# Kernel optimization log

Measured on AMD Instinct MI355X. Metric: run time of the kernel, lower is better.

## Reference

```python
import math
import jax, jax.numpy as jnp
import numpy as np

NUM_SUPERPIXELS = 256
COMPACTNESS = 10.0
NUM_ITERATIONS = 5


def _cdist(a, b):
    # Euclidean pairwise distance: a [B,N,C], b [B,K,C] -> [B,N,K]
    a2 = jnp.sum(a * a, axis=-1)[:, :, None]
    b2 = jnp.sum(b * b, axis=-1)[:, None, :]
    ab = jnp.einsum('bnc,bkc->bnk', a, b)
    return jnp.sqrt(jnp.maximum(a2 + b2 - 2.0 * ab, 1e-12))


def setup_inputs() -> dict:
    key = jax.random.key(0)
    x = jax.random.normal(key, (4, 200, 128, 128), dtype=jnp.float32)
    return {"x": x}


def reference(x):
    B, C, H, W = x.shape
    N = H * W

    # --- initialize_centers (grid of seed pixels, taken from x[0]) ---
    grid_h = int(math.sqrt(NUM_SUPERPIXELS * H / W))
    grid_w = NUM_SUPERPIXELS // grid_h
    K = grid_h * grid_w
    h_step, w_step = H // grid_h, W // grid_w
    h_idx = jnp.arange(h_step // 2, H, h_step)[:grid_h]
    w_idx = jnp.arange(w_step // 2, W, w_step)[:grid_w]
    gy, gx = jnp.meshgrid(h_idx, w_idx, indexing='ij')
    init_spatial = jnp.stack([gy.flatten(), gx.flatten()], axis=1).astype(jnp.float32)  # [K,2]
    flat_idx = gy.flatten() * W + gx.flatten()  # [K]

    # --- pixel coordinates ---
    yg, xg = jnp.meshgrid(jnp.arange(H), jnp.arange(W), indexing='ij')
    pix = jnp.stack([yg.flatten(), xg.flatten()], axis=1).astype(jnp.float32)  # [N,2]
    pix_b = jnp.broadcast_to(pix[None], (B, N, 2))

    x_flat = jnp.transpose(x, (0, 2, 3, 1)).reshape(B, N, C)  # [B,N,C]
    centers_spectral = jnp.broadcast_to(x_flat[0][flat_idx][None], (B, K, C))
    centers_spatial = jnp.broadcast_to(init_spatial[None], (B, K, 2))

    S = math.sqrt(H * W / NUM_SUPERPIXELS)
    Q = None
    for _ in range(NUM_ITERATIONS):
        D = _cdist(x_flat, centers_spectral) + (COMPACTNESS / S) * _cdist(pix_b, centers_spatial)
        Q = jax.nn.softmax(-D, axis=-1)  # [B,N,K]
        mass = jnp.sum(Q, axis=1)[:, :, None] + 1e-06  # [B,K,1]
        centers_spectral = jnp.einsum('bnk,bnc->bkc', Q, x_flat) / mass
        centers_spatial = jnp.einsum('bnk,bnc->bkc', Q, pix_b) / mass
    return Q, centers_spectral
```

## Files before the change

kernel.cpp:

```cpp
#include <hip/hip_runtime.h>
#include <math.h>

#define B 4
#define C 200
#define H 128
#define W 128
#define N 16384
#define K 256
#define ITERS 5
#define FACT 1.25f
#define NT 32
#define NTM 128
#define CPAD 208
#define CP2  224

typedef __attribute__((ext_vector_type(8))) __bf16 bf16x8;
typedef __attribute__((ext_vector_type(4))) float f32x4;

#define OFF_A2    0
#define OFF_CS    (OFF_A2 + B*N)
#define OFF_CSPAT (OFF_CS + B*K*C)
#define OFF_B2    (OFF_CSPAT + B*K*2)
#define OFF_SACC  (OFF_B2 + B*K)
#define OFF_MACC  (OFF_SACC + B*K*C)
#define OFF_SPACC (OFF_MACC + B*K)
#define OFF_CST   (OFF_SPACC + B*K*2)
#define CST_SZ    (B*C*K)
#define OFF_PART  (OFF_CST + CST_SZ)
#define PART_SZ   (B*NT*CPAD*K)
#define OFF_MPART (OFF_PART + PART_SZ)
#define MPART_SZ  (B*NTM*3*K)
#define WS_NEED   ((size_t)(OFF_MPART + MPART_SZ) * 4)
#define OFF_XBF   (OFF_MPART + MPART_SZ)
#define XBF_SZF   (B*N*CP2/2)
#define OFF_CSBF  (OFF_XBF + XBF_SZF)
#define CSBF_SZF  (B*K*CP2/2)
#define WS_NEED2  ((size_t)(OFF_CSBF + CSBF_SZF) * 4)

__global__ void k_init(const float* __restrict__ x, float* __restrict__ cs,
                       __bf16* __restrict__ csbf, float* __restrict__ cspat,
                       int fast) {
  int k = blockIdx.x, c = threadIdx.x;
  int i = k >> 4, j = k & 15;
  int sn = (4 + 8*i)*W + (4 + 8*j);
  if (c < C) {
    float v = x[(size_t)c*N + sn];
    for (int b = 0; b < B; ++b) {
      cs[((size_t)(b*K + k))*C + c] = v;
      if (fast) csbf[((size_t)(b*K + k))*CP2 + c] = (__bf16)v;
    }
  } else if (fast && c < CP2) {
    for (int b = 0; b < B; ++b)
      csbf[((size_t)(b*K + k))*CP2 + c] = (__bf16)0.f;
  }
  if (c == 0) {
    for (int b = 0; b < B; ++b) {
      cspat[(b*K + k)*2 + 0] = (float)(4 + 8*i);
      cspat[(b*K + k)*2 + 1] = (float)(4 + 8*j);
    }
  }
}

__global__ __launch_bounds__(256) void k_prep(const float* __restrict__ x,
                                              __bf16* __restrict__ xbf) {
  __shared__ float xt[32*64];
  int bid = blockIdx.x;
  int b  = bid >> 8;
  int n0 = (bid & 255) << 6;
  int tid = threadIdx.x;
  const float* xb = x + (size_t)b*C*N;
  __bf16* xo = xbf + ((size_t)b*N + n0)*CP2;
  for (int t = 0; t < 7; ++t) {
    int cc0 = t*32;
    __syncthreads();
    #pragma unroll
    for (int pass = 0; pass < 2; ++pass) {
      int f = pass*256 + tid;
      int ci = f >> 4, nq = f & 15;
      float4 v = make_float4(0.f, 0.f, 0.f, 0.f);
      if (cc0 + ci < C) v = *(const float4*)&xb[(size_t)(cc0 + ci)*N + n0 + nq*4];
      *(float4*)&xt[ci*64 + nq*4] = v;
    }
    __syncthreads();
    {
      int n = tid & 63, cg8 = (tid >> 6) * 8;
      bf16x8 pk;
      #pragma unroll
      for (int i = 0; i < 8; ++i) pk[i] = (__bf16)xt[(cg8 + i)*64 + n];
      *(bf16x8*)&xo[(size_t)n*CP2 + cc0 + cg8] = pk;
    }
  }
}

__global__ void k_a2(const float* __restrict__ x, float* __restrict__ a2) {
  int b = blockIdx.x >> 6;
  int n = ((blockIdx.x & 63) << 8) + threadIdx.x;
  const float* xp = x + (size_t)b*C*N + n;
  float s = 0.f;
  #pragma unroll 8
  for (int c = 0; c < C; ++c) { float v = xp[(size_t)c*N]; s += v*v; }
  a2[b*N + n] = s;
}

__global__ void k_b2(const float* __restrict__ cs, float* __restrict__ b2) {
  int bk = blockIdx.x;
  const float* p = cs + (size_t)bk*C;
  float s = 0.f;
  for (int c = threadIdx.x; c < C; c += 64) { float v = p[c]; s += v*v; }
  for (int off = 32; off > 0; off >>= 1) s += __shfl_down(s, off);
  if (threadIdx.x == 0) b2[bk] = s;
}

__global__ __launch_bounds__(512, 2) void k_assign2(
    const __bf16* __restrict__ xbf, const __bf16* __restrict__ csbf,
    const float* __restrict__ cspat, const float* __restrict__ b2,
    const float* __restrict__ a2, float* __restrict__ Q) {
  __shared__ float b2s[K], cys[K], cxs[K];
  __shared__ float a2s[128];
  __shared__ float redw[8*128];
  __shared__ float redf[128];

  int b   = blockIdx.x >> 7;
  int n0  = (blockIdx.x & 127) << 7;
  int tid = threadIdx.x;
  int lane = tid & 63;
  int lr = lane & 15;
  int lg = lane >> 4;
  int w  = tid >> 6;

  if (tid < K) {
    b2s[tid] = b2[b*K + tid];
    cys[tid] = cspat[(b*K + tid)*2 + 0];
    cxs[tid] = cspat[(b*K + tid)*2 + 1];
  }
  if (tid < 128) a2s[tid] = a2[b*N + n0 + tid];
  __syncthreads();

  f32x4 acc[16];
  #pragma unroll
  for (int i = 0; i < 16; ++i) acc[i] = (f32x4){0.f, 0.f, 0.f, 0.f};

  const __bf16* cb = csbf + ((size_t)b*K + (size_t)(w*32 + lr))*CP2;
  const __bf16* xb = xbf + ((size_t)(b*N + n0 + lr))*CP2;

  for (int t = 0; t < 7; ++t) {
    int cc = t*32 + lg*8;
    bf16x8 b0 = *(const bf16x8*)&cb[cc];
    bf16x8 b1 = *(const bf16x8*)&cb[(size_t)16*CP2 + cc];
    #pragma unroll
    for (int nt = 0; nt < 8; ++nt) {
      bf16x8 av = *(const bf16x8*)&xb[(size_t)(nt*16)*CP2 + cc];
      acc[nt*2+0] = __builtin_amdgcn_mfma_f32_16x16x32_bf16(av, b0, acc[nt*2+0], 0, 0, 0);
      acc[nt*2+1] = __builtin_amdgcn_mfma_f32_16x16x32_bf16(av, b1, acc[nt*2+1], 0, 0, 0);
    }
  }

  float py = (float)(n0 >> 7);
  int k0 = w*32 + lr, k1 = k0 + 16;
  float b2v0 = b2s[k0], b2v1 = b2s[k1];
  float cx0 = cxs[k0], cx1 = cxs[k1];
  float dy0 = py - cys[k0], dy1 = py - cys[k1];
  float dyy0 = dy0*dy0, dyy1 = dy1*dy1;

  float mArr[32];
  #pragma unroll
  for (int nt = 0; nt < 8; ++nt) {
    #pragma unroll
    for (int r = 0; r < 4; ++r) {
      int pix = nt*16 + lg*4 + r;
      float a2v = a2s[pix];
      float pxv = (float)pix;
      float dx0 = pxv - cx0, dx1 = pxv - cx1;
      float d0 = sqrtf(fmaxf(a2v + b2v0 - 2.f*acc[nt*2+0][r], 1e-12f))
               + FACT*sqrtf(fmaxf(dyy0 + dx0*dx0, 1e-12f));
      float d1 = sqrtf(fmaxf(a2v + b2v1 - 2.f*acc[nt*2+1][r], 1e-12f))
               + FACT*sqrtf(fmaxf(dyy1 + dx1*dx1, 1e-12f));
      float e0 = __expf(-d0);
      float e1 = __expf(-d1);
      acc[nt*2+0][r] = e0;
      acc[nt*2+1][r] = e1;
      float s = e0 + e1;
      s += __shfl_xor(s, 1);
      s += __shfl_xor(s, 2);
      s += __shfl_xor(s, 4);
      s += __shfl_xor(s, 8);
      mArr[nt*4+r] = s;
    }
  }
  if (lr == 0) {
    #pragma unroll
    for (int nt = 0; nt < 8; ++nt)
      #pragma unroll
      for (int r = 0; r < 4; ++r)
        redw[w*128 + nt*16 + lg*4 + r] = mArr[nt*4+r];
  }
  __syncthreads();
  if (tid < 128) {
    float s = redw[tid];
    #pragma unroll
    for (int g = 1; g < 8; ++g) s += redw[g*128 + tid];
    redf[tid] = 1.f / s;
  }
  __syncthreads();
  float* Qb = Q + ((size_t)(b*N + n0))*K;
  #pragma unroll
  for (int nt = 0; nt < 8; ++nt) {
    #pragma unroll
    for (int r = 0; r < 4; ++r) {
      int pix = nt*16 + lg*4 + r;
      float inv = redf[pix];
      Qb[(size_t)pix*K + k0] = acc[nt*2+0][r] * inv;
      Qb[(size_t)pix*K + k1] = acc[nt*2+1][r] * inv;
    }
  }
}

__global__ __launch_bounds__(512, 2) void k_assign(
    const float* __restrict__ x, const float* __restrict__ cs,
    const float* __restrict__ cspat, const float* __restrict__ b2,
    const float* __restrict__ a2, float* __restrict__ Q) {
  __shared__ __bf16 cs_lds[K*40];
  __shared__ __bf16 x_lds[128*40];
  __shared__ float b2s[K], cys[K], cxs[K];
  __shared__ float a2s[128];
  __shared__ float redw[8*128];
  __shared__ float redf[128];

  int b   = blockIdx.x >> 7;
  int n0  = (blockIdx.x & 127) << 7;
  int tid = threadIdx.x;
  int lane = tid & 63;
  int lr = lane & 15;
  int lg = lane >> 4;
  int w  = tid >> 6;

  if (tid < K) {
    b2s[tid] = b2[b*K + tid];
    cys[tid] = cspat[(b*K + tid)*2 + 0];
    cxs[tid] = cspat[(b*K + tid)*2 + 1];
  }
  if (tid < 128) a2s[tid] = a2[b*N + n0 + tid];

  f32x4 acc[16];
  #pragma unroll
  for (int i = 0; i < 16; ++i) acc[i] = (f32x4){0.f, 0.f, 0.f, 0.f};

  const float* xb = x + (size_t)b*C*N;
  const float* cb = cs + (size_t)b*K*C;

  for (int t = 0; t < 7; ++t) {
    int cc0 = t * 32;
    __syncthreads();
    #pragma unroll
    for (int pass = 0; pass < 4; ++pass) {
      int f = pass*512 + tid;
      int k = f >> 3, c4 = (f & 7) * 4;
      float4 v = make_float4(0.f, 0.f, 0.f, 0.f);
      if (cc0 + c4 < 200) v = *(const float4*)&cb[(size_t)k*C + cc0 + c4];
      __bf16* d = &cs_lds[k*40 + c4];
      d[0] = (__bf16)v.x; d[1] = (__bf16)v.y;
      d[2] = (__bf16)v.z; d[3] = (__bf16)v.w;
    }
    #pragma unroll
    for (int pass = 0; pass < 8; ++pass) {
      int idx = pass*512 + tid;
      int ci = idx >> 7, p = idx & 127;
      float xv = (cc0 + ci < 200) ? xb[(size_t)(cc0 + ci)*N + n0 + p] : 0.f;
      x_lds[p*40 + ci] = (__bf16)xv;
    }
    __syncthreads();
    const __bf16* bbase = &cs_lds[(w*32 + lr)*40 + lg*8];
    bf16x8 b0 = *(const bf16x8*)bbase;
    bf16x8 b1 = *(const bf16x8*)(bbase + 16*40);
    const __bf16* abase = &x_lds[lr*40 + lg*8];
    #pragma unroll
    for (int nt = 0; nt < 8; ++nt) {
      bf16x8 av = *(const bf16x8*)(abase + nt*16*40);
      acc[nt*2+0] = __builtin_amdgcn_mfma_f32_16x16x32_bf16(av, b0, acc[nt*2+0], 0, 0, 0);
      acc[nt*2+1] = __builtin_amdgcn_mfma_f32_16x16x32_bf16(av, b1, acc[nt*2+1], 0, 0, 0);
    }
  }

  float py = (float)(n0 >> 7);
  float mArr[32];
  #pragma unroll
  for (int nt = 0; nt < 8; ++nt) {
    #pragma unroll
    for (int r = 0; r < 4; ++r) {
      int pix = nt*16 + lg*4 + r;
      float a2v = a2s[pix];
      float pxv = (float)pix;
      float dmin = 1e30f;
      #pragma unroll
      for (int j = 0; j < 2; ++j) {
        int k = w*32 + j*16 + lr;
        float ab = acc[nt*2+j][r];
        float dy = py - cys[k];
        float dx = pxv - cxs[k];
        float d = sqrtf(fmaxf(a2v + b2s[k] - 2.f*ab, 1e-12f))
                + FACT*sqrtf(fmaxf(dy*dy + dx*dx, 1e-12f));
        acc[nt*2+j][r] = d;
        dmin = fminf(dmin, d);
      }
      mArr[nt*4+r] = dmin;
    }
  }
  #pragma unroll
  for (int i = 0; i < 32; ++i) {
    float m = mArr[i];
    m = fminf(m, __shfl_xor(m, 1));
    m = fminf(m, __shfl_xor(m, 2));
    m = fminf(m, __shfl_xor(m, 4));
    m = fminf(m, __shfl_xor(m, 8));
    mArr[i] = m;
  }
  if (lr == 0) {
    #pragma unroll
    for (int nt = 0; nt < 8; ++nt)
      #pragma unroll
      for (int r = 0; r < 4; ++r)
        redw[w*128 + nt*16 + lg*4 + r] = mArr[nt*4+r];
  }
  __syncthreads();
  if (tid < 128) {
    float m = redw[tid];
    #pragma unroll
    for (int g = 1; g < 8; ++g) m = fminf(m, redw[g*128 + tid]);
    redf[tid] = m;
  }
  __syncthreads();
  #pragma unroll
  for (int nt = 0; nt < 8; ++nt) {
    #pragma unroll
    for (int r = 0; r < 4; ++r) {
      int pix = nt*16 + lg*4 + r;
      float mnv = redf[pix];
      float s = 0.f;
      #pragma unroll
      for (int j = 0; j < 2; ++j) {
        float e = __expf(mnv - acc[nt*2+j][r]);
        acc[nt*2+j][r] = e;
        s += e;
      }
      s += __shfl_xor(s, 1);
      s += __shfl_xor(s, 2);
      s += __shfl_xor(s, 4);
      s += __shfl_xor(s, 8);
      mArr[nt*4+r] = s;
    }
  }
  if (lr == 0) {
    #pragma unroll
    for (int nt = 0; nt < 8; ++nt)
      #pragma unroll
      for (int r = 0; r < 4; ++r)
        redw[w*128 + nt*16 + lg*4 + r] = mArr[nt*4+r];
  }
  __syncthreads();
  if (tid < 128) {
    float s = redw[tid];
    #pragma unroll
    for (int g = 1; g < 8; ++g) s += redw[g*128 + tid];
    redf[tid] = 1.f / s;
  }
  __syncthreads();
  float* Qb = Q + ((size_t)(b*N + n0))*K;
  #pragma unroll
  for (int nt = 0; nt < 8; ++nt) {
    #pragma unroll
    for (int r = 0; r < 4; ++r) {
      int pix = nt*16 + lg*4 + r;
      float inv = redf[pix];
      #pragma unroll
      for (int j = 0; j < 2; ++j) {
        int k = w*32 + j*16 + lr;
        Qb[(size_t)pix*K + k] = acc[nt*2+j][r] * inv;
      }
    }
  }
}

__global__ __launch_bounds__(256) void k_update4(
    const float* __restrict__ x, const float* __restrict__ Q,
    float* __restrict__ part) {
  __shared__ float  q32[32*256];
  __shared__ __bf16 qbf[256*40];
  __shared__ __bf16 xbf[64*40];
  int bid = blockIdx.x;
  int b   = bid >> 7;
  int rem = bid & 127;
  int cg  = rem >> 5;
  int nt  = rem & 31;
  int tid = threadIdx.x;
  int lane = tid & 63, lr = lane & 15, lg = lane >> 4;
  int w   = tid >> 6;
  int c0  = cg * 64;

  f32x4 acc[16];
  #pragma unroll
  for (int i = 0; i < 16; ++i) acc[i] = (f32x4){0.f, 0.f, 0.f, 0.f};

  const float* Qb = Q + (size_t)b*N*K;
  const float* xb = x + (size_t)b*C*N;

  for (int ch = 0; ch < 16; ++ch) {
    int nb = nt*512 + ch*32;
    __syncthreads();
    #pragma unroll
    for (int pass = 0; pass < 8; ++pass) {
      int f = pass*256 + tid;
      int n = f >> 6, k4 = f & 63;
      *(float4*)&q32[n*256 + k4*4] =
          *(const float4*)&Qb[(size_t)(nb + n)*K + k4*4];
    }
    #pragma unroll
    for (int pass = 0; pass < 2; ++pass) {
      int f = pass*256 + tid;
      int c = f >> 3, n4 = f & 7;
      int cc = c0 + c;
      float4 v = make_float4(0.f, 0.f, 0.f, 0.f);
      if (cc < 200) v = *(const float4*)&xb[(size_t)cc*N + nb + n4*4];
      __bf16* d = &xbf[c*40 + n4*4];
      d[0] = (__bf16)v.x; d[1] = (__bf16)v.y;
      d[2] = (__bf16)v.z; d[3] = (__bf16)v.w;
    }
    __syncthreads();
    {
      #pragma unroll
      for (int g = 0; g < 4; ++g) {
        bf16x8 pk;
        #pragma unroll
        for (int i = 0; i < 8; ++i)
          pk[i] = (__bf16)q32[(g*8 + i)*256 + tid];
        *(bf16x8*)&qbf[tid*40 + g*8] = pk;
      }
    }
    __syncthreads();
    const __bf16* abase = &qbf[(w*64 + lr)*40 + lg*8];
    const __bf16* bbase = &xbf[lr*40 + lg*8];
    bf16x8 A0 = *(const bf16x8*)(abase);
    bf16x8 A1 = *(const bf16x8*)(abase + 16*40);
    bf16x8 A2 = *(const bf16x8*)(abase + 32*40);
    bf16x8 A3 = *(const bf16x8*)(abase + 48*40);
    bf16x8 B0 = *(const bf16x8*)(bbase);
    bf16x8 B1 = *(const bf16x8*)(bbase + 16*40);
    bf16x8 B2 = *(const bf16x8*)(bbase + 32*40);
    bf16x8 B3 = *(const bf16x8*)(bbase + 48*40);
    acc[0]  = __builtin_amdgcn_mfma_f32_16x16x32_bf16(A0, B0, acc[0], 0, 0, 0);
    acc[1]  = __builtin_amdgcn_mfma_f32_16x16x32_bf16(A0, B1, acc[1], 0, 0, 0);
    acc[2]  = __builtin_amdgcn_mfma_f32_16x16x32_bf16(A0, B2, acc[2], 0, 0, 0);
    acc[3]  = __builtin_amdgcn_mfma_f32_16x16x32_bf16(A0, B3, acc[3], 0, 0, 0);
    acc[4]  = __builtin_amdgcn_mfma_f32_16x16x32_bf16(A1, B0, acc[4], 0, 0, 0);
    acc[5]  = __builtin_amdgcn_mfma_f32_16x16x32_bf16(A1, B1, acc[5], 0, 0, 0);
    acc[6]  = __builtin_amdgcn_mfma_f32_16x16x32_bf16(A1, B2, acc[6], 0, 0, 0);
    acc[7]  = __builtin_amdgcn_mfma_f32_16x16x32_bf16(A1, B3, acc[7], 0, 0, 0);
    acc[8]  = __builtin_amdgcn_mfma_f32_16x16x32_bf16(A2, B0, acc[8], 0, 0, 0);
    acc[9]  = __builtin_amdgcn_mfma_f32_16x16x32_bf16(A2, B1, acc[9], 0, 0, 0);
    acc[10] = __builtin_amdgcn_mfma_f32_16x16x32_bf16(A2, B2, acc[10], 0, 0, 0);
    acc[11] = __builtin_amdgcn_mfma_f32_16x16x32_bf16(A2, B3, acc[11], 0, 0, 0);
    acc[12] = __builtin_amdgcn_mfma_f32_16x16x32_bf16(A3, B0, acc[12], 0, 0, 0);
    acc[13] = __builtin_amdgcn_mfma_f32_16x16x32_bf16(A3, B1, acc[13], 0, 0, 0);
    acc[14] = __builtin_amdgcn_mfma_f32_16x16x32_bf16(A3, B2, acc[14], 0, 0, 0);
    acc[15] = __builtin_amdgcn_mfma_f32_16x16x32_bf16(A3, B3, acc[15], 0, 0, 0);
  }

  float* pp = part + (size_t)(b*NT + nt) * CPAD * K;
  #pragma unroll
  for (int t = 0; t < 4; ++t) {
    #pragma unroll
    for (int u = 0; u < 4; ++u) {
      int c = c0 + u*16 + lr;
      if (c < CPAD) {
        int k = w*64 + t*16 + lg*4;
        *(f32x4*)&pp[(size_t)c*K + k] = acc[t*4+u];
      }
    }
  }
}

__global__ __launch_bounds__(256) void k_mass(
    const float* __restrict__ Q, float* __restrict__ mpart) {
  int bid = blockIdx.x;
  int b = bid >> 7, nt = bid & 127;
  int tid = threadIdx.x;
  const float* Qb = Q + (size_t)b*N*K;
  int nbase = nt * 128;
  float mass = 0.f, sy = 0.f, sx = 0.f;
  for (int nn = 0; nn < 128; nn += 8) {
    float qv[8];
    #pragma unroll
    for (int j = 0; j < 8; ++j)
      qv[j] = Qb[(size_t)(nbase + nn + j)*K + tid];
    #pragma unroll
    for (int j = 0; j < 8; ++j) {
      int n = nbase + nn + j;
      mass += qv[j];
      sy += qv[j] * (float)(n >> 7);
      sx += qv[j] * (float)(n & 127);
    }
  }
  float* mp = mpart + (size_t)(b*NTM + nt) * 3 * K;
  mp[tid]       = mass;
  mp[K + tid]   = sy;
  mp[2*K + tid] = sx;
}

__global__ __launch_bounds__(256) void k_reduce(
    const float* __restrict__ part, const float* __restrict__ mpart,
    float* __restrict__ sacc, float* __restrict__ macc,
    float* __restrict__ spacc) {
  int bid = blockIdx.x;
  int b = bid / 200;
  int c = bid % 200;
  int tid = threadIdx.x;
  float s = 0.f;
  for (int nt = 0; nt < NT; ++nt)
    s += part[((size_t)(b*NT + nt)*CPAD + c)*K + tid];
  sacc[(size_t)(b*K + tid)*C + c] = s;
  if (c == 0) {
    float m = 0.f, yy = 0.f, xx = 0.f;
    for (int nt = 0; nt < NTM; ++nt) {
      const float* mp = mpart + (size_t)(b*NTM + nt) * 3 * K;
      m  += mp[tid];
      yy += mp[K + tid];
      xx += mp[2*K + tid];
    }
    macc[b*K + tid] = m;
    spacc[(b*K + tid)*2 + 0] = yy;
    spacc[(b*K + tid)*2 + 1] = xx;
  }
}

__global__ __launch_bounds__(256, 2) void k_update(
    const float* __restrict__ x, const float* __restrict__ Q,
    float* __restrict__ sacc, float* __restrict__ macc,
    float* __restrict__ spacc) {
  __shared__ float x_lds[32*28];
  int bid = blockIdx.x;
  int b = bid >> 9;
  int rest = bid & 511;
  int ct = rest >> 6;
  int nt = rest & 63;
  int tid = threadIdx.x;
  int c0 = ct * 25;

  float acc[25];
  #pragma unroll
  for (int c = 0; c < 25; ++c) acc[c] = 0.f;
  float mass = 0.f, sy = 0.f, sx = 0.f;

  const float* xb = x + (size_t)b*C*N + (size_t)c0*N;
  const float* Qb = Q + (size_t)b*N*K;

  for (int ch = 0; ch < 8; ++ch) {
    int nb = nt*256 + ch*32;
    __syncthreads();
    #pragma unroll
    for (int pass = 0; pass < 4; ++pass) {
      int idx = pass*256 + tid;
      if (idx < 800) {
        int ci = idx >> 5, nn = idx & 31;
        x_lds[nn*28 + ci] = xb[(size_t)ci*N + nb + nn];
      }
    }
    __syncthreads();
    float py  = (float)(nb >> 7);
    float pxb = (float)(nb & 127);
    #pragma unroll
    for (int n4 = 0; n4 < 8; ++n4) {
      float qv[4];
      #pragma unroll
      for (int j = 0; j < 4; ++j)
        qv[j] = Qb[(size_t)(nb + n4*4 + j)*K + tid];
      #pragma unroll
      for (int j = 0; j < 4; ++j) {
        int nn = n4*4 + j;
        float q = qv[j];
        if (ct == 0) {
          mass += q;
          sy += q * py;
          sx += q * (pxb + (float)nn);
        }
        const float* xr = &x_lds[nn*28];
        #pragma unroll
        for (int c4 = 0; c4 < 6; ++c4) {
          float4 xv = *(const float4*)&xr[c4*4];
          acc[c4*4+0] = fmaf(q, xv.x, acc[c4*4+0]);
          acc[c4*4+1] = fmaf(q, xv.y, acc[c4*4+1]);
          acc[c4*4+2] = fmaf(q, xv.z, acc[c4*4+2]);
          acc[c4*4+3] = fmaf(q, xv.w, acc[c4*4+3]);
        }
        acc[24] = fmaf(q, xr[24], acc[24]);
      }
    }
  }
  float* sp = sacc + ((size_t)(b*K + tid))*C + c0;
  #pragma unroll
  for (int c = 0; c < 25; ++c) atomicAdd(&sp[c], acc[c]);
  if (ct == 0) {
    atomicAdd(&macc[b*K + tid], mass);
    atomicAdd(&spacc[(b*K + tid)*2 + 0], sy);
    atomicAdd(&spacc[(b*K + tid)*2 + 1], sx);
  }
}

__global__ void k_final(const float* __restrict__ sacc, const float* __restrict__ macc,
                        const float* __restrict__ spacc, float* __restrict__ cs,
                        __bf16* __restrict__ csbf, float* __restrict__ cspat,
                        float* __restrict__ b2, float* __restrict__ outc,
                        int last, int fast) {
  __shared__ float red[256];
  int bk = blockIdx.x;
  int c = threadIdx.x;
  float inv = 1.f / (macc[bk] + 1e-6f);
  float v = 0.f;
  if (c < C) {
    v = sacc[(size_t)bk*C + c] * inv;
    cs[(size_t)bk*C + c] = v;
    if (fast) csbf[(size_t)bk*CP2 + c] = (__bf16)v;
    if (last) outc[(size_t)bk*C + c] = v;
  } else if (c == C) {
    cspat[bk*2 + 0] = spacc[bk*2 + 0] * inv;
  } else if (c == C + 1) {
    cspat[bk*2 + 1] = spacc[bk*2 + 1] * inv;
  }
  red[c] = v * v;
  __syncthreads();
  for (int off = 128; off > 0; off >>= 1) {
    if (c < off) red[c] += red[c + off];
    __syncthreads();
  }
  if (c == 0) b2[bk] = red[0];
}

extern "C" void kernel_launch(void* const* d_in, const int* in_sizes, int n_in,
                              void* d_out, int out_size, void* d_ws, size_t ws_size,
                              hipStream_t stream) {
  const float* x = (const float*)d_in[0];
  float* out = (float*)d_out;
  float* ws  = (float*)d_ws;
  float* a2    = ws + OFF_A2;
  float* cs    = ws + OFF_CS;
  float* cspat = ws + OFF_CSPAT;
  float* b2    = ws + OFF_B2;
  float* sacc  = ws + OFF_SACC;
  float* macc  = ws + OFF_MACC;
  float* spacc = ws + OFF_SPACC;
  float* part  = ws + OFF_PART;
  float* mpart = ws + OFF_MPART;
  __bf16* xbf  = (__bf16*)(ws + OFF_XBF);
  __bf16* csbf = (__bf16*)(ws + OFF_CSBF);
  float* outc  = out + (size_t)B*N*K;
  int split = (ws_size >= WS_NEED) ? 1 : 0;
  int fast  = (ws_size >= WS_NEED2) ? 1 : 0;

  hipLaunchKernelGGL(k_init, dim3(K), dim3(256), 0, stream, x, cs, csbf, cspat, fast);
  hipLaunchKernelGGL(k_a2, dim3(B*64), dim3(256), 0, stream, x, a2);
  hipLaunchKernelGGL(k_b2, dim3(B*K), dim3(64), 0, stream, cs, b2);
  if (fast)
    hipLaunchKernelGGL(k_prep, dim3(B*256), dim3(256), 0, stream, x, xbf);
  for (int it = 0; it < ITERS; ++it) {
    if (fast)
      hipLaunchKernelGGL(k_assign2, dim3(B*128), dim3(512), 0, stream,
                         xbf, csbf, cspat, b2, a2, out);
    else
      hipLaunchKernelGGL(k_assign, dim3(B*128), dim3(512), 0, stream,
                         x, cs, cspat, b2, a2, out);
    if (split) {
      hipLaunchKernelGGL(k_update4, dim3(B*4*NT), dim3(256), 0, stream,
                         x, out, part);
      hipLaunchKernelGGL(k_mass, dim3(B*NTM), dim3(256), 0, stream,
                         out, mpart);
      hipLaunchKernelGGL(k_reduce, dim3(B*200), dim3(256), 0, stream,
                         part, mpart, sacc, macc, spacc);
    } else {
      hipMemsetAsync(sacc, 0, (size_t)(B*K*C + B*K + B*K*2)*sizeof(float), stream);
      hipLaunchKernelGGL(k_update, dim3(B*512), dim3(256), 0, stream,
                         x, out, sacc, macc, spacc);
    }
    hipLaunchKernelGGL(k_final, dim3(B*K), dim3(256), 0, stream,
                       sacc, macc, spacc, cs, csbf, cspat, b2, outc,
                       (it == ITERS-1) ? 1 : 0, fast);
  }
}
```

Before: 624.4 us.

## Emit transposed bf16 Q from assign and feed a direct-load MFMA update kernel

The assign kernel now also writes a K-major bf16 copy of Q, and a new prep kernel converts x once into a channel-major bf16 buffer padded to CPAD. A new update kernel then runs the Q^T·x reduction with MFMA, loading operands straight from these pre-laid-out global buffers with no LDS staging or on-the-fly conversion. This is meant to cut the fp32 read and convert cost of the update step. In exchange it adds extra workspace and extra bf16 stores in assign, and the new path only runs if the workspace is large enough.

```diff
diff --git a/kernel.cpp b/kernel.cpp
--- a/kernel.cpp
+++ b/kernel.cpp
@@ -15,6 +15,7 @@
 #define CP2  224
 
 typedef __attribute__((ext_vector_type(8))) __bf16 bf16x8;
+typedef __attribute__((ext_vector_type(4))) __bf16 bf16x4;
 typedef __attribute__((ext_vector_type(4))) float f32x4;
 
 #define OFF_A2    0
@@ -36,6 +37,11 @@
 #define OFF_CSBF  (OFF_XBF + XBF_SZF)
 #define CSBF_SZF  (B*K*CP2/2)
 #define WS_NEED2  ((size_t)(OFF_CSBF + CSBF_SZF) * 4)
+#define OFF_QTB   (OFF_CSBF + CSBF_SZF)
+#define QTB_SZF   (B*K*N/2)
+#define OFF_XB2   (OFF_QTB + QTB_SZF)
+#define XB2_SZF   (B*CPAD*N/2)
+#define WS_NEED3  ((size_t)(OFF_XB2 + XB2_SZF) * 4)
 
 __global__ void k_init(const float* __restrict__ x, float* __restrict__ cs,
                        __bf16* __restrict__ csbf, float* __restrict__ cspat,
@@ -92,6 +98,28 @@
   }
 }
 
+__global__ __launch_bounds__(256) void k_prep2(const float* __restrict__ x,
+                                               __bf16* __restrict__ xbf2) {
+  int g = blockIdx.x * 256 + threadIdx.x;
+  int per_b = CPAD * (N/8);
+  int b = g / per_b;
+  int rem = g - b*per_b;
+  int c = rem / (N/8);
+  int n = (rem - c*(N/8)) * 8;
+  bf16x8 pk;
+  if (c < C) {
+    const float* src = &x[((size_t)b*C + c)*N + n];
+    float4 v0 = *(const float4*)&src[0];
+    float4 v1 = *(const float4*)&src[4];
+    pk[0]=(__bf16)v0.x; pk[1]=(__bf16)v0.y; pk[2]=(__bf16)v0.z; pk[3]=(__bf16)v0.w;
+    pk[4]=(__bf16)v1.x; pk[5]=(__bf16)v1.y; pk[6]=(__bf16)v1.z; pk[7]=(__bf16)v1.w;
+  } else {
+    #pragma unroll
+    for (int i = 0; i < 8; ++i) pk[i] = (__bf16)0.f;
+  }
+  *(bf16x8*)&xbf2[((size_t)b*CPAD + c)*N + n] = pk;
+}
+
 __global__ void k_a2(const float* __restrict__ x, float* __restrict__ a2) {
   int b = blockIdx.x >> 6;
   int n = ((blockIdx.x & 63) << 8) + threadIdx.x;
@@ -114,7 +142,8 @@
 __global__ __launch_bounds__(512, 2) void k_assign2(
     const __bf16* __restrict__ xbf, const __bf16* __restrict__ csbf,
     const float* __restrict__ cspat, const float* __restrict__ b2,
-    const float* __restrict__ a2, float* __restrict__ Q) {
+    const float* __restrict__ a2, float* __restrict__ Q,
+    __bf16* __restrict__ qtb, int wq) {
   __shared__ float b2s[K], cys[K], cxs[K];
   __shared__ float a2s[128];
   __shared__ float redw[8*128];
@@ -203,14 +232,25 @@
   }
   __syncthreads();
   float* Qb = Q + ((size_t)(b*N + n0))*K;
+  __bf16* qt0 = qtb + ((size_t)b*K + k0)*N + n0;
+  __bf16* qt1 = qtb + ((size_t)b*K + k1)*N + n0;
   #pragma unroll
   for (int nt = 0; nt < 8; ++nt) {
+    bf16x4 p0, p1;
     #pragma unroll
     for (int r = 0; r < 4; ++r) {
       int pix = nt*16 + lg*4 + r;
       float inv = redf[pix];
-      Qb[(size_t)pix*K + k0] = acc[nt*2+0][r] * inv;
-      Qb[(size_t)pix*K + k1] = acc[nt*2+1][r] * inv;
+      float f0 = acc[nt*2+0][r] * inv;
+      float f1 = acc[nt*2+1][r] * inv;
+      Qb[(size_t)pix*K + k0] = f0;
+      Qb[(size_t)pix*K + k1] = f1;
+      p0[r] = (__bf16)f0;
+      p1[r] = (__bf16)f1;
+    }
+    if (wq) {
+      *(bf16x4*)&qt0[nt*16 + lg*4] = p0;
+      *(bf16x4*)&qt1[nt*16 + lg*4] = p1;
     }
   }
 }
@@ -375,6 +415,75 @@
       for (int j = 0; j < 2; ++j) {
         int k = w*32 + j*16 + lr;
         Qb[(size_t)pix*K + k] = acc[nt*2+j][r] * inv;
+      }
+    }
+  }
+}
+
+__global__ __launch_bounds__(256) void k_update5(
+    const __bf16* __restrict__ qtb, const __bf16* __restrict__ xbf2,
+    float* __restrict__ part) {
+  int bid = blockIdx.x;
+  int b   = bid >> 7;
+  int rem = bid & 127;
+  int cg  = rem >> 5;
+  int nt  = rem & 31;
+  int tid = threadIdx.x;
+  int lane = tid & 63, lr = lane & 15, lg = lane >> 4;
+  int w   = tid >> 6;
+  int c0  = cg * 64;
+
+  f32x4 acc[16];
+  #pragma unroll
+  for (int i = 0; i < 16; ++i) acc[i] = (f32x4){0.f, 0.f, 0.f, 0.f};
+
+  const __bf16* qb = qtb + ((size_t)b*K + (size_t)(w*64 + lr))*N;
+  int cr0 = c0 + lr;
+  int cr1 = min(c0 + 16 + lr, CPAD - 1);
+  int cr2 = min(c0 + 32 + lr, CPAD - 1);
+  int cr3 = min(c0 + 48 + lr, CPAD - 1);
+  const __bf16* xb0 = xbf2 + ((size_t)b*CPAD + cr0)*N;
+  const __bf16* xb1 = xbf2 + ((size_t)b*CPAD + cr1)*N;
+  const __bf16* xb2 = xbf2 + ((size_t)b*CPAD + cr2)*N;
+  const __bf16* xb3 = xbf2 + ((size_t)b*CPAD + cr3)*N;
+
+  for (int ch = 0; ch < 16; ++ch) {
+    int nb = nt*512 + ch*32 + lg*8;
+    bf16x8 A0 = *(const bf16x8*)&qb[nb];
+    bf16x8 A1 = *(const bf16x8*)&qb[(size_t)16*N + nb];
+    bf16x8 A2 = *(const bf16x8*)&qb[(size_t)32*N + nb];
+    bf16x8 A3 = *(const bf16x8*)&qb[(size_t)48*N + nb];
+    bf16x8 B0 = *(const bf16x8*)&xb0[nb];
+    bf16x8 B1 = *(const bf16x8*)&xb1[nb];
+    bf16x8 B2 = *(const bf16x8*)&xb2[nb];
+    bf16x8 B3 = *(const bf16x8*)&xb3[nb];
+    acc[0]  = __builtin_amdgcn_mfma_f32_16x16x32_bf16(A0, B0, acc[0], 0, 0, 0);
+    acc[1]  = __builtin_amdgcn_mfma_f32_16x16x32_bf16(A0, B1, acc[1], 0, 0, 0);
+    acc[2]  = __builtin_amdgcn_mfma_f32_16x16x32_bf16(A0, B2, acc[2], 0, 0, 0);
+    acc[3]  = __builtin_amdgcn_mfma_f32_16x16x32_bf16(A0, B3, acc[3], 0, 0, 0);
+    acc[4]  = __builtin_amdgcn_mfma_f32_16x16x32_bf16(A1, B0, acc[4], 0, 0, 0);
+    acc[5]  = __builtin_amdgcn_mfma_f32_16x16x32_bf16(A1, B1, acc[5], 0, 0, 0);
+    acc[6]  = __builtin_amdgcn_mfma_f32_16x16x32_bf16(A1, B2, acc[6], 0, 0, 0);
+    acc[7]  = __builtin_amdgcn_mfma_f32_16x16x32_bf16(A1, B3, acc[7], 0, 0, 0);
+    acc[8]  = __builtin_amdgcn_mfma_f32_16x16x32_bf16(A2, B0, acc[8], 0, 0, 0);
+    acc[9]  = __builtin_amdgcn_mfma_f32_16x16x32_bf16(A2, B1, acc[9], 0, 0, 0);
+    acc[10] = __builtin_amdgcn_mfma_f32_16x16x32_bf16(A2, B2, acc[10], 0, 0, 0);
+    acc[11] = __builtin_amdgcn_mfma_f32_16x16x32_bf16(A2, B3, acc[11], 0, 0, 0);
+    acc[12] = __builtin_amdgcn_mfma_f32_16x16x32_bf16(A3, B0, acc[12], 0, 0, 0);
+    acc[13] = __builtin_amdgcn_mfma_f32_16x16x32_bf16(A3, B1, acc[13], 0, 0, 0);
+    acc[14] = __builtin_amdgcn_mfma_f32_16x16x32_bf16(A3, B2, acc[14], 0, 0, 0);
+    acc[15] = __builtin_amdgcn_mfma_f32_16x16x32_bf16(A3, B3, acc[15], 0, 0, 0);
+  }
+
+  float* pp = part + (size_t)(b*NT + nt) * CPAD * K;
+  #pragma unroll
+  for (int t = 0; t < 4; ++t) {
+    #pragma unroll
+    for (int u = 0; u < 4; ++u) {
+      int c = c0 + u*16 + lr;
+      if (c < CPAD) {
+        int k = w*64 + t*16 + lg*4;
+        *(f32x4*)&pp[(size_t)c*K + k] = acc[t*4+u];
       }
     }
   }
@@ -650,25 +759,34 @@
   float* mpart = ws + OFF_MPART;
   __bf16* xbf  = (__bf16*)(ws + OFF_XBF);
   __bf16* csbf = (__bf16*)(ws + OFF_CSBF);
+  __bf16* qtb  = (__bf16*)(ws + OFF_QTB);
+  __bf16* xbf2 = (__bf16*)(ws + OFF_XB2);
   float* outc  = out + (size_t)B*N*K;
   int split = (ws_size >= WS_NEED) ? 1 : 0;
   int fast  = (ws_size >= WS_NEED2) ? 1 : 0;
+  int fast2 = (ws_size >= WS_NEED3) ? 1 : 0;
 
   hipLaunchKernelGGL(k_init, dim3(K), dim3(256), 0, stream, x, cs, csbf, cspat, fast);
   hipLaunchKernelGGL(k_a2, dim3(B*64), dim3(256), 0, stream, x, a2);
   hipLaunchKernelGGL(k_b2, dim3(B*K), dim3(64), 0, stream, cs, b2);
   if (fast)
     hipLaunchKernelGGL(k_prep, dim3(B*256), dim3(256), 0, stream, x, xbf);
+  if (fast2)
+    hipLaunchKernelGGL(k_prep2, dim3(B*CPAD*N/8/256), dim3(256), 0, stream, x, xbf2);
   for (int it = 0; it < ITERS; ++it) {
     if (fast)
       hipLaunchKernelGGL(k_assign2, dim3(B*128), dim3(512), 0, stream,
-                         xbf, csbf, cspat, b2, a2, out);
+                         xbf, csbf, cspat, b2, a2, out, qtb, fast2);
     else
       hipLaunchKernelGGL(k_assign, dim3(B*128), dim3(512), 0, stream,
                          x, cs, cspat, b2, a2, out);
     if (split) {
-      hipLaunchKernelGGL(k_update4, dim3(B*4*NT), dim3(256), 0, stream,
-                         x, out, part);
+      if (fast2)
+        hipLaunchKernelGGL(k_update5, dim3(B*4*NT), dim3(256), 0, stream,
+                           qtb, xbf2, part);
+      else
+        hipLaunchKernelGGL(k_update4, dim3(B*4*NT), dim3(256), 0, stream,
+                           x, out, part);
       hipLaunchKernelGGL(k_mass, dim3(B*NTM), dim3(256), 0, stream,
                          out, mpart);
       hipLaunchKernelGGL(k_reduce, dim3(B*200), dim3(256), 0, stream,
```

Result: slower. 646.7 us (+3.6%).
